# Performance work log

Measured on AMD Instinct MI355X. Metric: run time of the kernel, lower is better.

Reference implementation:

```python
import jax, jax.numpy as jnp
import numpy as np

N_NODES = 100000


def _gcn_layer(x, W, b, src, dst, edge_weight):
    # GCNConv with normalize=False: linear transform, then weighted scatter-add
    h = x @ W                                   # [N, out]
    msg = h[src] * edge_weight[:, None]         # gather source features, scale per edge
    agg = jax.ops.segment_sum(msg, dst, num_segments=N_NODES)  # scatter-add to destinations
    return agg + b


def setup_inputs() -> dict:
    key = jax.random.key(0)
    k = jax.random.split(key, 6)
    N, F_in, H, C, E = N_NODES, 256, 16, 40, 3200000
    x = jax.random.normal(k[0], (N, F_in), dtype=jnp.float32)
    edge_index = jax.random.randint(k[1], (2, E), 0, N, dtype=jnp.int64)
    edge_weight = jax.random.uniform(k[2], (E,), dtype=jnp.float32)
    # Glorot-style init for weights
    W1 = jax.random.normal(k[3], (F_in, H), dtype=jnp.float32) * (1.0 / np.sqrt(F_in))
    b1 = jnp.zeros((H,), dtype=jnp.float32)
    W2 = jax.random.normal(k[4], (H, C), dtype=jnp.float32) * (1.0 / np.sqrt(H))
    b2 = jnp.zeros((C,), dtype=jnp.float32)
    return {"x": x, "edge_index": edge_index, "edge_weight": edge_weight,
            "W1": W1, "b1": b1, "W2": W2, "b2": b2}


def reference(x, edge_index, edge_weight, W1, b1, W2, b2):
    src, dst = edge_index[0], edge_index[1]
    h = jax.nn.relu(_gcn_layer(x, W1, b1, src, dst, edge_weight))
    # dropout is identity in eval mode
    h = _gcn_layer(h, W2, b2, src, dst, edge_weight)
    return jax.nn.log_softmax(h, axis=1)
```

## Files before the change

### kernel.cpp

```cpp
#include <hip/hip_runtime.h>
#include <hip/hip_bf16.h>
#include <cstdint>

#define F_IN 256
#define F_H  16
#define F_P  8
#define F_C  40

__global__ __launch_bounds__(256) void gemm1_kernel(
    const float* __restrict__ x, const float* __restrict__ W1,
    __hip_bfloat162* __restrict__ t1, int N) {
  __shared__ float wlds[F_IN * F_H];
  __shared__ float xlds[16 * 260];
  const int tid = threadIdx.x;
  const int nodeBase = blockIdx.x * 16;

  for (int i = tid; i < F_IN * F_H; i += 256) wlds[i] = W1[i];

  const float4* x4 = reinterpret_cast<const float4*>(x) + (size_t)nodeBase * (F_IN / 4);
  for (int i = tid; i < 16 * (F_IN / 4); i += 256) {
    int r = i >> 6;
    int c4 = i & 63;
    float4 v = make_float4(0.f, 0.f, 0.f, 0.f);
    if (nodeBase + r < N) v = x4[(size_t)r * (F_IN / 4) + c4];
    *reinterpret_cast<float4*>(&xlds[r * 260 + c4 * 4]) = v;
  }
  __syncthreads();

  const int r = tid >> 4;
  const int f = tid & 15;
  const float* xr = &xlds[r * 260];
  float acc = 0.f;
#pragma unroll 8
  for (int k = 0; k < F_IN; ++k) acc = fmaf(xr[k], wlds[k * F_H + f], acc);

  float hi = __shfl_down(acc, 1);
  if (((f & 1) == 0) && (nodeBase + r < N)) {
    __hip_bfloat162 h2 = __halves2bfloat162(__float2bfloat16(acc), __float2bfloat16(hi));
    t1[(size_t)(nodeBase + r) * F_P + (f >> 1)] = h2;
  }
}

__global__ __launch_bounds__(256) void scatter1_kernel(
    const __hip_bfloat162* __restrict__ t1, const int* __restrict__ ei,
    const float* __restrict__ ew, __hip_bfloat162* __restrict__ agg1,
    int N, int E) {
  int gid = blockIdx.x * 256 + threadIdx.x;
  int e = gid >> 3;
  int p = gid & 7;
  if (e >= E) return;
  int s = ei[e];
  int d = ei[E + e];
  if ((unsigned)s >= (unsigned)N || (unsigned)d >= (unsigned)N) return;
  float w = ew[e];
  __hip_bfloat162 tv = t1[(size_t)s * F_P + p];
  __hip_bfloat162 v = __halves2bfloat162(
      __float2bfloat16(__bfloat162float(tv.x) * w),
      __float2bfloat16(__bfloat162float(tv.y) * w));
  unsafeAtomicAdd(&agg1[(size_t)d * F_P + p], v);
}

__global__ __launch_bounds__(256) void scatter2_kernel(
    const __hip_bfloat162* __restrict__ agg1, const float* __restrict__ b1,
    const int* __restrict__ ei, const float* __restrict__ ew,
    __hip_bfloat162* __restrict__ agg2, int N, int E) {
  int gid = blockIdx.x * 256 + threadIdx.x;
  int e = gid >> 3;
  int p = gid & 7;
  if (e >= E) return;
  int s = ei[e];
  int d = ei[E + e];
  if ((unsigned)s >= (unsigned)N || (unsigned)d >= (unsigned)N) return;
  float w = ew[e];
  __hip_bfloat162 av = agg1[(size_t)s * F_P + p];
  float lo = __bfloat162float(av.x) + b1[2 * p];
  float hi = __bfloat162float(av.y) + b1[2 * p + 1];
  lo = lo > 0.f ? lo * w : 0.f;
  hi = hi > 0.f ? hi * w : 0.f;
  __hip_bfloat162 v = __halves2bfloat162(__float2bfloat16(lo), __float2bfloat16(hi));
  unsafeAtomicAdd(&agg2[(size_t)d * F_P + p], v);
}

__global__ __launch_bounds__(320) void gemm2_lsm_kernel(
    const __hip_bfloat162* __restrict__ agg2, const float* __restrict__ W2,
    const float* __restrict__ b2, float* __restrict__ out, int N) {
  __shared__ float w2lds[F_H * F_C];
  __shared__ float alds[8 * F_H];
  __shared__ float slds[8 * F_C];
  __shared__ float mlog[8];
  const int tid = threadIdx.x;
  const int nodeBase = blockIdx.x * 8;

  for (int i = tid; i < F_H * F_C; i += 320) w2lds[i] = W2[i];
  if (tid < 8 * F_P) {
    int node = nodeBase + (tid >> 3);
    __hip_bfloat162 v{};
    if (node < N) v = agg2[(size_t)nodeBase * F_P + tid];
    int r = tid >> 3, p = tid & 7;
    alds[r * F_H + 2 * p]     = __bfloat162float(v.x);
    alds[r * F_H + 2 * p + 1] = __bfloat162float(v.y);
  }
  __syncthreads();

  const int ln = tid / F_C;
  const int c = tid - ln * F_C;
  float acc = b2[c];
#pragma unroll
  for (int k = 0; k < F_H; ++k) acc = fmaf(alds[ln * F_H + k], w2lds[k * F_C + c], acc);
  slds[tid] = acc;
  __syncthreads();

  if (tid < 8) {
    const float* row = &slds[tid * F_C];
    float m = -INFINITY;
#pragma unroll
    for (int f = 0; f < F_C; ++f) m = fmaxf(m, row[f]);
    float s = 0.f;
#pragma unroll
    for (int f = 0; f < F_C; ++f) s += expf(row[f] - m);
    mlog[tid] = m + logf(s);
  }
  __syncthreads();

  const int node = nodeBase + ln;
  if (node < N) out[(size_t)nodeBase * F_C + tid] = slds[tid] - mlog[ln];
}

extern "C" void kernel_launch(void* const* d_in, const int* in_sizes, int n_in,
                              void* d_out, int out_size, void* d_ws, size_t ws_size,
                              hipStream_t stream) {
  const float* x  = (const float*)d_in[0];
  const int*   ei = (const int*)d_in[1];
  const float* ew = (const float*)d_in[2];
  const float* W1 = (const float*)d_in[3];
  const float* b1 = (const float*)d_in[4];
  const float* W2 = (const float*)d_in[5];
  const float* b2 = (const float*)d_in[6];
  float* out = (float*)d_out;

  const int N = in_sizes[0] / F_IN;
  const int E = in_sizes[2];

  __hip_bfloat162* t1   = (__hip_bfloat162*)d_ws;
  __hip_bfloat162* agg1 = t1 + (size_t)N * F_P;
  __hip_bfloat162* agg2 = agg1 + (size_t)N * F_P;

  hipMemsetAsync(agg1, 0, (size_t)N * F_P * 2 * sizeof(__hip_bfloat162), stream);

  gemm1_kernel<<<(N + 15) / 16, 256, 0, stream>>>(x, W1, t1, N);
  scatter1_kernel<<<((size_t)E * F_P + 255) / 256, 256, 0, stream>>>(t1, ei, ew, agg1, N, E);
  scatter2_kernel<<<((size_t)E * F_P + 255) / 256, 256, 0, stream>>>(agg1, b1, ei, ew, agg2, N, E);
  gemm2_lsm_kernel<<<(N + 7) / 8, 320, 0, stream>>>(agg2, W2, b2, out, N);
}
```

Measured before the change: 552.9 us.

## Transpose W1 in LDS and compute two nodes per thread with float4 reads

The first GEMM kernel now stores W1 transposed in LDS with padding. Each thread reads float4 vectors of W and x and accumulates two node rows that share the same weights. Each block covers 32 nodes instead of 16, which halves the number of blocks and halves the per-node cost of loading W1 into LDS. LDS use per block rises, which may lower occupancy. The GEMM is likely a small share of total time next to the two scatter kernels.

```diff
diff --git a/kernel.cpp b/kernel.cpp
--- a/kernel.cpp
+++ b/kernel.cpp
@@ -6,38 +6,56 @@
 #define F_H  16
 #define F_P  8
 #define F_C  40
+#define XS   32
 
 __global__ __launch_bounds__(256) void gemm1_kernel(
     const float* __restrict__ x, const float* __restrict__ W1,
     __hip_bfloat162* __restrict__ t1, int N) {
-  __shared__ float wlds[F_IN * F_H];
-  __shared__ float xlds[16 * 260];
+  __shared__ float xlds[XS * 260];
+  __shared__ float wlds[F_H * 260];
   const int tid = threadIdx.x;
-  const int nodeBase = blockIdx.x * 16;
+  const int nodeBase = blockIdx.x * XS;
 
-  for (int i = tid; i < F_IN * F_H; i += 256) wlds[i] = W1[i];
-
+  for (int i = tid; i < F_IN * F_H; i += 256) {
+    int k = i >> 4, f = i & 15;
+    wlds[f * 260 + k] = W1[i];
+  }
   const float4* x4 = reinterpret_cast<const float4*>(x) + (size_t)nodeBase * (F_IN / 4);
-  for (int i = tid; i < 16 * (F_IN / 4); i += 256) {
-    int r = i >> 6;
-    int c4 = i & 63;
+  for (int i = tid; i < XS * (F_IN / 4); i += 256) {
+    int r = i >> 6, c4 = i & 63;
     float4 v = make_float4(0.f, 0.f, 0.f, 0.f);
     if (nodeBase + r < N) v = x4[(size_t)r * (F_IN / 4) + c4];
     *reinterpret_cast<float4*>(&xlds[r * 260 + c4 * 4]) = v;
   }
   __syncthreads();
 
-  const int r = tid >> 4;
-  const int f = tid & 15;
-  const float* xr = &xlds[r * 260];
-  float acc = 0.f;
+  const int r0 = tid >> 4;
+  const int f  = tid & 15;
+  const float4* xa = reinterpret_cast<const float4*>(&xlds[r0 * 260]);
+  const float4* xb = reinterpret_cast<const float4*>(&xlds[(r0 + 16) * 260]);
+  const float4* wf = reinterpret_cast<const float4*>(&wlds[f * 260]);
+  float acca = 0.f, accb = 0.f;
 #pragma unroll 8
-  for (int k = 0; k < F_IN; ++k) acc = fmaf(xr[k], wlds[k * F_H + f], acc);
+  for (int k4 = 0; k4 < F_IN / 4; ++k4) {
+    float4 w = wf[k4];
+    float4 a = xa[k4];
+    float4 b = xb[k4];
+    acca = fmaf(a.x, w.x, acca); acca = fmaf(a.y, w.y, acca);
+    acca = fmaf(a.z, w.z, acca); acca = fmaf(a.w, w.w, acca);
+    accb = fmaf(b.x, w.x, accb); accb = fmaf(b.y, w.y, accb);
+    accb = fmaf(b.z, w.z, accb); accb = fmaf(b.w, w.w, accb);
+  }
 
-  float hi = __shfl_down(acc, 1);
-  if (((f & 1) == 0) && (nodeBase + r < N)) {
-    __hip_bfloat162 h2 = __halves2bfloat162(__float2bfloat16(acc), __float2bfloat16(hi));
-    t1[(size_t)(nodeBase + r) * F_P + (f >> 1)] = h2;
+  float hia = __shfl_down(acca, 1);
+  float hib = __shfl_down(accb, 1);
+  if ((f & 1) == 0) {
+    int p = f >> 1;
+    if (nodeBase + r0 < N)
+      t1[(size_t)(nodeBase + r0) * F_P + p] =
+          __halves2bfloat162(__float2bfloat16(acca), __float2bfloat16(hia));
+    if (nodeBase + r0 + 16 < N)
+      t1[(size_t)(nodeBase + r0 + 16) * F_P + p] =
+          __halves2bfloat162(__float2bfloat16(accb), __float2bfloat16(hib));
   }
 }
 
@@ -147,7 +165,7 @@
 
   hipMemsetAsync(agg1, 0, (size_t)N * F_P * 2 * sizeof(__hip_bfloat162), stream);
 
-  gemm1_kernel<<<(N + 15) / 16, 256, 0, stream>>>(x, W1, t1, N);
+  gemm1_kernel<<<(N + XS - 1) / XS, 256, 0, stream>>>(x, W1, t1, N);
   scatter1_kernel<<<((size_t)E * F_P + 255) / 256, 256, 0, stream>>>(t1, ei, ew, agg1, N, E);
   scatter2_kernel<<<((size_t)E * F_P + 255) / 256, 256, 0, stream>>>(agg1, b1, ei, ew, agg2, N, E);
   gemm2_lsm_kernel<<<(N + 7) / 8, 320, 0, stream>>>(agg2, W2, b2, out, N);
```

After: 550.2 us. No clear change (-0.5%).
